# Performance work log

Hardware: AMD Instinct MI355X
Metric: run time of the kernel (lower is better)

Reference implementation:

```python
import jax, jax.numpy as jnp
import numpy as np

NUM_HEADS = 16


def setup_inputs() -> dict:
    key = jax.random.key(0)
    ks = jax.random.split(key, 5)
    b, s, d = 2, 2048, 1024
    std = (2.0 / (d + d)) ** 0.5
    x = jax.random.normal(ks[0], (b, s, d), dtype=jnp.float32)
    Wq = jax.random.normal(ks[1], (d, d), dtype=jnp.float32) * std
    Wk = jax.random.normal(ks[2], (d, d), dtype=jnp.float32) * std
    Wv = jax.random.normal(ks[3], (d, d), dtype=jnp.float32) * std
    Wo = jax.random.normal(ks[4], (d, d), dtype=jnp.float32) * std
    return {"x": x, "Wq": Wq, "Wk": Wk, "Wv": Wv, "Wo": Wo}


def reference(x, Wq, Wk, Wv, Wo):
    b, s, d = x.shape
    h = NUM_HEADS
    dk = d // h
    # projections: bias-free x @ W (W is [in, out])
    def split_heads(t):
        return t.reshape(b, s, h, dk).transpose(0, 2, 1, 3)  # b h s dk
    q = split_heads(x @ Wq)
    k = split_heads(x @ Wk)
    v = split_heads(x @ Wv)
    scale = 1.0 / jnp.sqrt(jnp.asarray(dk, dtype=x.dtype))
    scores = jnp.einsum('bhqd,bhkd->bhqk', q, k) * scale  # b h s s
    causal = jnp.tril(jnp.ones((s, s), dtype=bool))
    scores = jnp.where(causal, scores, -jnp.inf)
    probs = jax.nn.softmax(scores, axis=-1)
    out = jnp.einsum('bhqk,bhkd->bhqd', probs, v)
    out = out.transpose(0, 2, 1, 3).reshape(b, s, d)  # b s (h dk)
    return out @ Wo
```

## Files before the change

### kernel.cpp

```cpp
#include <hip/hip_runtime.h>

typedef unsigned short u16;
typedef unsigned int   u32;

using bf16x8 = __attribute__((ext_vector_type(8))) __bf16;
using bf16x4 = __attribute__((ext_vector_type(4))) __bf16;
using f32x4  = __attribute__((ext_vector_type(4))) float;
using s16x4  = __attribute__((ext_vector_type(4))) short;

#define NH    16
#define DKH   64
#define SEQ   2048
#define BAT   2
#define DMOD  1024

#define QSCALE 0.18033688011112042f

__device__ __forceinline__ u16 f2bf(float f) {
  union { float f; u32 u; } v; v.f = f;
  u32 r = v.u + 0x7fffu + ((v.u >> 16) & 1u);
  return (u16)(r >> 16);
}

__device__ __forceinline__ u32 pack2bf(float a, float b) {
  union { float f; u32 u; } x, y; x.f = a; y.f = b;
  u32 ua = x.u + 0x7fffu + ((x.u >> 16) & 1u);
  u32 ub = y.u + 0x7fffu + ((y.u >> 16) & 1u);
  return __builtin_amdgcn_perm(ub, ua, 0x07060302u);
}

__device__ __forceinline__ s16x4 pk4bf(float a, float b, float c, float d) {
  union { bf16x4 bv; s16x4 sv; } u;
  u.bv[0] = (__bf16)a; u.bv[1] = (__bf16)b; u.bv[2] = (__bf16)c; u.bv[3] = (__bf16)d;
  return u.sv;
}

#if __has_builtin(__builtin_amdgcn_exp2f)
#define EXP2(x) __builtin_amdgcn_exp2f(x)
#else
#define EXP2(x) exp2f(x)
#endif

#if __has_builtin(__builtin_amdgcn_mfma_f32_16x16x16bf16_1k)
__device__ __forceinline__ f32x4 mfma16(s16x4 a, s16x4 b, f32x4 c) {
  return __builtin_amdgcn_mfma_f32_16x16x16bf16_1k(a, b, c, 0, 0, 0);
}
#else
__device__ __forceinline__ f32x4 mfma16(s16x4 a, s16x4 b, f32x4 c) {
  f32x4 d;
  asm volatile("v_mfma_f32_16x16x16_bf16 %0, %1, %2, %3\n\ts_nop 7\n\ts_nop 7"
               : "=v"(d) : "v"(a), "v"(b), "v"(c));
  return d;
}
#endif

typedef const __attribute__((address_space(1))) u32 glb_u32;
typedef __attribute__((address_space(3))) u32 lds_u32;
__device__ __forceinline__ void gload16(const u16* g, u16* l) {
  __builtin_amdgcn_global_load_lds((glb_u32*)(const void*)g, (lds_u32*)(void*)l, 16, 0, 0);
}

__global__ __launch_bounds__(256) void transpose_all(const float* __restrict__ Wq,
                                                     const float* __restrict__ Wk,
                                                     const float* __restrict__ Wv,
                                                     const float* __restrict__ Wo,
                                                     u16* __restrict__ Wt) {
  __shared__ u16 t[32][33];
  const float* W = blockIdx.z == 0 ? Wq : blockIdx.z == 1 ? Wk : blockIdx.z == 2 ? Wv : Wo;
  u16* o = Wt + (size_t)blockIdx.z * DMOD * DMOD;
  int bx = blockIdx.x * 32, by = blockIdx.y * 32;
  int x = threadIdx.x, y = threadIdx.y;
  #pragma unroll
  for (int i = 0; i < 32; i += 8)
    t[y + i][x] = f2bf(W[(size_t)(by + y + i) * DMOD + bx + x]);
  __syncthreads();
  #pragma unroll
  for (int i = 0; i < 32; i += 8)
    o[(size_t)(bx + y + i) * DMOD + by + x] = t[x][y + i];
}

__global__ __launch_bounds__(256) void convert_x(const float* __restrict__ x,
                                                 u16* __restrict__ xb) {
  size_t i = ((size_t)blockIdx.x * 256 + threadIdx.x) * 8;
  float4 f0 = *(const float4*)(x + i);
  float4 f1 = *(const float4*)(x + i + 4);
  uint4 o;
  o.x = pack2bf(f0.x, f0.y); o.y = pack2bf(f0.z, f0.w);
  o.z = pack2bf(f1.x, f1.y); o.w = pack2bf(f1.z, f1.w);
  *(uint4*)(xb + i) = o;
}

__global__ __launch_bounds__(256, 3) void gemm_qkv(const u16* __restrict__ A,
                                                   const u16* __restrict__ Bt,
                                                   u16* __restrict__ Qo,
                                                   u16* __restrict__ Ko,
                                                   u16* __restrict__ Vo) {
  __shared__ __align__(16) u16 As[128 * 32];
  __shared__ __align__(16) u16 Bs[128 * 32];
  const int tid  = threadIdx.x;
  const int lane = tid & 63, wv = tid >> 6;
  const int wm   = wv >> 1, wn = wv & 1;
  const int lrow = lane & 15, quad = lane >> 4;
  const int tileM = blockIdx.x * 128, tileN = blockIdx.y * 128;

  const f32x4 fz = {0.f, 0.f, 0.f, 0.f};
  f32x4 acc[4][4];
  #pragma unroll
  for (int i = 0; i < 4; ++i)
    #pragma unroll
    for (int j = 0; j < 4; ++j) acc[i][j] = fz;

  for (int kt = 0; kt < DMOD; kt += 32) {
    if (kt) __syncthreads();
    #pragma unroll
    for (int i = 0; i < 2; ++i) {
      int idx = i * 256 + tid;
      gload16(&A [(size_t)(tileM + (idx >> 2)) * DMOD + kt + (idx & 3) * 8], &As[idx * 8]);
      gload16(&Bt[(size_t)(tileN + (idx >> 2)) * DMOD + kt + (idx & 3) * 8], &Bs[idx * 8]);
    }
    __syncthreads();

    bf16x8 af[4], bfr[4];
    #pragma unroll
    for (int mt = 0; mt < 4; ++mt)
      af[mt] = *(const bf16x8*)(&As[(wm * 64 + mt * 16 + lrow) * 32 + quad * 8]);
    #pragma unroll
    for (int nt = 0; nt < 4; ++nt)
      bfr[nt] = *(const bf16x8*)(&Bs[(wn * 64 + nt * 16 + lrow) * 32 + quad * 8]);
    #pragma unroll
    for (int mt = 0; mt < 4; ++mt)
      #pragma unroll
      for (int nt = 0; nt < 4; ++nt)
        acc[mt][nt] = __builtin_amdgcn_mfma_f32_16x16x32_bf16(af[mt], bfr[nt],
                                                              acc[mt][nt], 0, 0, 0);
  }

  #pragma unroll
  for (int mt = 0; mt < 4; ++mt) {
    #pragma unroll
    for (int nt = 0; nt < 4; ++nt) {
      int gm0 = tileM + wm * 64 + mt * 16 + quad * 4;
      int gn  = tileN + wn * 64 + nt * 16 + lrow;
      int which = gn >> 10, col = gn & 1023;
      int bb = gm0 >> 11, srw0 = gm0 & (SEQ - 1);
      int hh = col >> 6, dki = col & (DKH - 1);
      size_t bhi = (size_t)(bb * NH + hh);
      if (which == 0) {
        #pragma unroll
        for (int r = 0; r < 4; ++r)
          Qo[(bhi * SEQ + srw0 + r) * DKH + dki] = f2bf(acc[mt][nt][r] * QSCALE);
      } else if (which == 1) {
        #pragma unroll
        for (int r = 0; r < 4; ++r)
          Ko[(bhi * SEQ + srw0 + r) * DKH + dki] = f2bf(acc[mt][nt][r]);
      } else {
        uint2 pk;
        pk.x = pack2bf(acc[mt][nt][0], acc[mt][nt][1]);
        pk.y = pack2bf(acc[mt][nt][2], acc[mt][nt][3]);
        *(uint2*)(&Vo[(((bhi * (SEQ / 4)) + (srw0 >> 2)) * DKH + dki) * 4]) = pk;
      }
    }
  }
}

__global__ __launch_bounds__(256, 3) void gemm_out(const u16* __restrict__ A,
                                                   const u16* __restrict__ Bt,
                                                   float* __restrict__ Co) {
  __shared__ __align__(16) u16 As[128 * 32];
  __shared__ __align__(16) u16 Bs[64 * 32];
  const int tid  = threadIdx.x;
  const int lane = tid & 63, wv = tid >> 6;
  const int wm   = wv & 1, wn = wv >> 1;
  const int lrow = lane & 15, quad = lane >> 4;
  const int tileM = blockIdx.x * 128, tileN = blockIdx.y * 64;

  const f32x4 fz = {0.f, 0.f, 0.f, 0.f};
  f32x4 acc[4][2];
  #pragma unroll
  for (int i = 0; i < 4; ++i) { acc[i][0] = fz; acc[i][1] = fz; }

  for (int kt = 0; kt < DMOD; kt += 32) {
    if (kt) __syncthreads();
    #pragma unroll
    for (int i = 0; i < 2; ++i) {
      int idx = i * 256 + tid;
      gload16(&A[(size_t)(tileM + (idx >> 2)) * DMOD + kt + (idx & 3) * 8], &As[idx * 8]);
    }
    gload16(&Bt[(size_t)(tileN + (tid >> 2)) * DMOD + kt + (tid & 3) * 8], &Bs[tid * 8]);
    __syncthreads();

    bf16x8 af[4], bfr[2];
    #pragma unroll
    for (int mt = 0; mt < 4; ++mt)
      af[mt] = *(const bf16x8*)(&As[(wm * 64 + mt * 16 + lrow) * 32 + quad * 8]);
    #pragma unroll
    for (int nt = 0; nt < 2; ++nt)
      bfr[nt] = *(const bf16x8*)(&Bs[(wn * 32 + nt * 16 + lrow) * 32 + quad * 8]);
    #pragma unroll
    for (int mt = 0; mt < 4; ++mt)
      #pragma unroll
      for (int nt = 0; nt < 2; ++nt)
        acc[mt][nt] = __builtin_amdgcn_mfma_f32_16x16x32_bf16(af[mt], bfr[nt],
                                                              acc[mt][nt], 0, 0, 0);
  }

  #pragma unroll
  for (int mt = 0; mt < 4; ++mt)
    #pragma unroll
    for (int nt = 0; nt < 2; ++nt)
      #pragma unroll
      for (int r = 0; r < 4; ++r) {
        int gm = tileM + wm * 64 + mt * 16 + quad * 4 + r;
        int gn = tileN + wn * 32 + nt * 16 + lrow;
        Co[(size_t)gm * DMOD + gn] = acc[mt][nt][r];
      }
}

#define OPAD 68

__global__ __launch_bounds__(256, 2) void attn_k(const u16* __restrict__ Q,
                                                 const u16* __restrict__ Kg,
                                                 const u16* __restrict__ Vg,
                                                 u16* __restrict__ Og) {
  __shared__ __align__(16) u16 Ksb[2][2][64 * 64];
  __shared__ __align__(16) u16 Vsb[2][2][16 * 256];
  __shared__ __align__(16) u16 Osc[64 * OPAD];
  __shared__ float Lsc[32];

  const int tid  = threadIdx.x;
  const int lane = tid & 63, w = tid >> 6;
  const int g    = w >> 1,  wg = w & 1;
  const int lrow = lane & 15, quad = lane >> 4;
  const int bh = blockIdx.x, y = blockIdx.y;
  const int b = bh >> 4, h = bh & 15;
  const int qB = 31 - y;
  const int sAend = y >> 1;

  const u16* Qbh = Q  + (size_t)bh * SEQ * DKH;
  const u16* Kbh = Kg + (size_t)bh * SEQ * DKH;
  const u16* Vbh = Vg + (size_t)bh * SEQ * DKH;

  const f32x4 fz = {0.f, 0.f, 0.f, 0.f};
  f32x4 oacc[2][4];
  float lsum[2];
  bf16x8 bq[2][2];

#define DEC(s_, g_, qt_, j_, v_)                                                   \
  { if ((s_) <= sAend) { qt_ = y;  j_ = 2 * (s_) + (g_);              v_ = (j_ <= y);  } \
    else               { qt_ = qB; j_ = 2 * ((s_) - sAend - 1) + (g_); v_ = (j_ <= qB); } }

#define STAGE1(gg, p_, j_)                                                          \
  { _Pragma("unroll")                                                               \
    for (int i_ = 0; i_ < 2; ++i_) {                                                \
      int cD = i_ * 256 + tid; int r_ = cD >> 3, c_ = cD & 7;                       \
      gload16(&Kbh[(size_t)((j_) * 64 + r_) * DKH + ((c_ ^ (r_ & 7)) << 3)],        \
              &Ksb[gg][p_][cD * 8]); }                                              \
    _Pragma("unroll")                                                               \
    for (int i_ = 0; i_ < 2; ++i_) {                                                \
      int cD = i_ * 256 + tid; int sq_ = cD >> 5, c_ = cD & 31;                     \
      gload16(&Vbh[(size_t)((j_) * 16 + sq_) * 256 + ((c_ ^ (sq_ & 7)) << 3)],      \
              &Vsb[gg][p_][cD * 8]); } }

#define LOADQ(qt_)                                                                  \
  { _Pragma("unroll")                                                               \
    for (int s_ = 0; s_ < 2; ++s_)                                                  \
      _Pragma("unroll")                                                             \
      for (int kk_ = 0; kk_ < 2; ++kk_)                                             \
        bq[s_][kk_] = *(const bf16x8*)(&Qbh[(size_t)((qt_) * 64 + wg * 32 + s_ * 16 \
                                            + lrow) * DKH + kk_ * 32 + quad * 8]); }

  auto EPI = [&](int qt) {
    float ls[2];
    #pragma unroll
    for (int s2 = 0; s2 < 2; ++s2) {
      float v = lsum[s2];
      v += __shfl_xor(v, 16, 64);
      v += __shfl_xor(v, 32, 64);
      ls[s2] = v;
    }
    float* OscF = (float*)Osc;
    #pragma unroll
    for (int ph = 0; ph < 2; ++ph) {
      if (g == 1) {
        int srow = wg * 16 + lrow;
        #pragma unroll
        for (int d = 0; d < 4; ++d)
          *(f32x4*)(&OscF[srow * OPAD + d * 16 + quad * 4]) = oacc[ph][d];
        if (quad == 0) Lsc[srow] = ls[ph];
      }
      __syncthreads();
      if (g == 0) {
        int srow = wg * 16 + lrow;
        ls[ph] += Lsc[srow];
        #pragma unroll
        for (int d = 0; d < 4; ++d) {
          f32x4 ov = *(const f32x4*)(&OscF[srow * OPAD + d * 16 + quad * 4]);
          oacc[ph][d] += ov;
        }
      }
      __syncthreads();
    }
    if (g == 0) {
      #pragma unroll
      for (int s2 = 0; s2 < 2; ++s2) {
        float inv = 1.f / ls[s2];
        int row = wg * 32 + s2 * 16 + lrow;
        #pragma unroll
        for (int d = 0; d < 4; ++d) {
          uint2 pkk;
          pkk.x = pack2bf(oacc[s2][d][0] * inv, oacc[s2][d][1] * inv);
          pkk.y = pack2bf(oacc[s2][d][2] * inv, oacc[s2][d][3] * inv);
          *(uint2*)(&Osc[row * OPAD + d * 16 + quad * 4]) = pkk;
        }
      }
    }
    __syncthreads();
    #pragma unroll
    for (int k2 = 0; k2 < 2; ++k2) {
      int c2 = k2 * 256 + tid;
      int row = c2 >> 3, ch = c2 & 7;
      uint4 vv = *(const uint4*)(&Osc[row * OPAD + ch * 8]);
      *(uint4*)(&Og[(size_t)(b * SEQ + qt * 64 + row) * DMOD + h * DKH + ch * 8]) = vv;
    }
  };

  { int qt0, j0; bool v0;
    DEC(0, 0, qt0, j0, v0); if (v0) STAGE1(0, 0, j0);
    DEC(0, 1, qt0, j0, v0); if (v0) STAGE1(1, 0, j0);
  }
  LOADQ(y);
  #pragma unroll
  for (int s2 = 0; s2 < 2; ++s2) {
    oacc[s2][0] = fz; oacc[s2][1] = fz; oacc[s2][2] = fz; oacc[s2][3] = fz;
    lsum[s2] = 0.f;
  }
  __syncthreads();

  for (int s = 0; s <= 16; ++s) {
    const int p = s & 1;

    if (s < 16) {
      int qtn, jn; bool vn;
      DEC(s + 1, 0, qtn, jn, vn); if (vn) STAGE1(0, p ^ 1, jn);
      DEC(s + 1, 1, qtn, jn, vn); if (vn) STAGE1(1, p ^ 1, jn);
    }

    int qt, j; bool valid;
    DEC(s, g, qt, j, valid);
    if (valid) {
      const u16* Ks = Ksb[g][p];
      const u16* Vs = Vsb[g][p];
      if (j < qt) {
        __builtin_amdgcn_s_setprio(1);
        f32x4 sacc[2][4];
        #pragma unroll
        for (int s2 = 0; s2 < 2; ++s2)
          #pragma unroll
          for (int m = 0; m < 4; ++m) sacc[s2][m] = fz;
        #pragma unroll
        for (int kk = 0; kk < 2; ++kk)
          #pragma unroll
          for (int m = 0; m < 4; ++m) {
            bf16x8 ak = *(const bf16x8*)(&Ks[(m * 16 + lrow) * 64
                                             + (((kk * 4 + quad) ^ (lrow & 7)) << 3)]);
            sacc[0][m] = __builtin_amdgcn_mfma_f32_16x16x32_bf16(ak, bq[0][kk], sacc[0][m], 0, 0, 0);
            sacc[1][m] = __builtin_amdgcn_mfma_f32_16x16x32_bf16(ak, bq[1][kk], sacc[1][m], 0, 0, 0);
          }
        #pragma unroll
        for (int m = 0; m < 4; ++m) {
          float p00 = EXP2(sacc[0][m][0]), p01 = EXP2(sacc[0][m][1]);
          float p02 = EXP2(sacc[0][m][2]), p03 = EXP2(sacc[0][m][3]);
          float p10 = EXP2(sacc[1][m][0]), p11 = EXP2(sacc[1][m][1]);
          float p12 = EXP2(sacc[1][m][2]), p13 = EXP2(sacc[1][m][3]);
          lsum[0] += (p00 + p01) + (p02 + p03);
          lsum[1] += (p10 + p11) + (p12 + p13);
          s16x4 pk0 = pk4bf(p00, p01, p02, p03);
          s16x4 pk1 = pk4bf(p10, p11, p12, p13);
          const int sq = m * 4 + quad;
          #pragma unroll
          for (int d = 0; d < 4; ++d) {
            int dk = d * 16 + lrow;
            s16x4 av = *(const s16x4*)(&Vs[sq * 256
                                           + ((((dk >> 1) ^ (sq & 7)) << 3) | ((dk & 1) << 2))]);
            oacc[0][d] = mfma16(av, pk0, oacc[0][d]);
            oacc[1][d] = mfma16(av, pk1, oacc[1][d]);
          }
        }
        __builtin_amdgcn_s_setprio(0);
      } else {
        #pragma unroll
        for (int s2 = 0; s2 < 2; ++s2) {
          const int L = 2 * wg + s2;
          for (int m = 0; m < L; ++m) {
            f32x4 sv = fz;
            #pragma unroll
            for (int kk = 0; kk < 2; ++kk) {
              bf16x8 ak = *(const bf16x8*)(&Ks[(m * 16 + lrow) * 64
                                               + (((kk * 4 + quad) ^ (lrow & 7)) << 3)]);
              sv = __builtin_amdgcn_mfma_f32_16x16x32_bf16(ak, bq[s2][kk], sv, 0, 0, 0);
            }
            float p0 = EXP2(sv[0]), p1 = EXP2(sv[1]), p2 = EXP2(sv[2]), p3 = EXP2(sv[3]);
            lsum[s2] += (p0 + p1) + (p2 + p3);
            s16x4 pk = pk4bf(p0, p1, p2, p3);
            const int sq = m * 4 + quad;
            #pragma unroll
            for (int d = 0; d < 4; ++d) {
              int dk = d * 16 + lrow;
              s16x4 av = *(const s16x4*)(&Vs[sq * 256
                                             + ((((dk >> 1) ^ (sq & 7)) << 3) | ((dk & 1) << 2))]);
              oacc[s2][d] = mfma16(av, pk, oacc[s2][d]);
            }
          }
          {
            f32x4 sv = fz;
            #pragma unroll
            for (int kk = 0; kk < 2; ++kk) {
              bf16x8 ak = *(const bf16x8*)(&Ks[(L * 16 + lrow) * 64
                                               + (((kk * 4 + quad) ^ (lrow & 7)) << 3)]);
              sv = __builtin_amdgcn_mfma_f32_16x16x32_bf16(ak, bq[s2][kk], sv, 0, 0, 0);
            }
            float pp[4];
            #pragma unroll
            for (int r = 0; r < 4; ++r)
              pp[r] = (quad * 4 + r > lrow) ? 0.f : EXP2(sv[r]);
            lsum[s2] += (pp[0] + pp[1]) + (pp[2] + pp[3]);
            s16x4 pk = pk4bf(pp[0], pp[1], pp[2], pp[3]);
            const int sq = L * 4 + quad;
            #pragma unroll
            for (int d = 0; d < 4; ++d) {
              int dk = d * 16 + lrow;
              s16x4 av = *(const s16x4*)(&Vs[sq * 256
                                             + ((((dk >> 1) ^ (sq & 7)) << 3) | ((dk & 1) << 2))]);
              oacc[s2][d] = mfma16(av, pk, oacc[s2][d]);
            }
          }
        }
      }
    }

    __syncthreads();

    if (s == sAend) {
      EPI(y);
      #pragma unroll
      for (int s2 = 0; s2 < 2; ++s2) {
        oacc[s2][0] = fz; oacc[s2][1] = fz; oacc[s2][2] = fz; oacc[s2][3] = fz;
        lsum[s2] = 0.f;
      }
      LOADQ(qB);
    } else if (s == 16) {
      EPI(qB);
    }
  }
#undef DEC
#undef STAGE1
#undef LOADQ
}

extern "C" void kernel_launch(void* const* d_in, const int* in_sizes, int n_in,
                              void* d_out, int out_size, void* d_ws, size_t ws_size,
                              hipStream_t stream) {
  const float* x  = (const float*)d_in[0];
  const float* Wq = (const float*)d_in[1];
  const float* Wk = (const float*)d_in[2];
  const float* Wv = (const float*)d_in[3];
  const float* Wo = (const float*)d_in[4];

  u16* ws = (u16*)d_ws;
  const size_t WSZ = (size_t)DMOD * DMOD;
  const size_t TSZ = (size_t)BAT * NH * SEQ * DKH;
  u16* Wt  = ws;
  u16* Wto = Wt + 3 * WSZ;
  u16* xb  = Wt + 4 * WSZ;
  u16* Qb  = xb + TSZ;
  u16* Kb  = Qb + TSZ;
  u16* Vb  = Kb + TSZ;
  u16* Ob  = xb;

  transpose_all<<<dim3(32, 32, 4), dim3(32, 8), 0, stream>>>(Wq, Wk, Wv, Wo, Wt);
  convert_x<<<dim3(2048), 256, 0, stream>>>(x, xb);

  gemm_qkv<<<dim3(32, 24), 256, 0, stream>>>(xb, Wt, Qb, Kb, Vb);

  attn_k<<<dim3(32, 16), 256, 0, stream>>>(Qb, Kb, Vb, Ob);

  gemm_out<<<dim3(32, 16), 256, 0, stream>>>(Ob, Wto, (float*)d_out);
}
```

Baseline: 170.4 us.

## Double GEMM K-tile to 64 with XOR-swizzled LDS layout

Both projection GEMMs now stage 64-wide K slices in shared memory instead of 32, which halves the number of barrier pairs per tile. The LDS layout gains an XOR swizzle on the 16-byte chunk index, applied on global load and on fragment read, to avoid bank conflicts on the wider rows. LDS use per block doubles, which may limit occupancy relative to the launch bound of 3 blocks.

Result: faster. 164.4 us (-3.5%).

```diff
diff --git a/kernel.cpp b/kernel.cpp
--- a/kernel.cpp
+++ b/kernel.cpp
@@ -95,8 +95,8 @@
                                                    u16* __restrict__ Qo,
                                                    u16* __restrict__ Ko,
                                                    u16* __restrict__ Vo) {
-  __shared__ __align__(16) u16 As[128 * 32];
-  __shared__ __align__(16) u16 Bs[128 * 32];
+  __shared__ __align__(16) u16 As[128 * 64];
+  __shared__ __align__(16) u16 Bs[128 * 64];
   const int tid  = threadIdx.x;
   const int lane = tid & 63, wv = tid >> 6;
   const int wm   = wv >> 1, wn = wv & 1;
@@ -110,29 +110,35 @@
     #pragma unroll
     for (int j = 0; j < 4; ++j) acc[i][j] = fz;
 
-  for (int kt = 0; kt < DMOD; kt += 32) {
+  for (int kt = 0; kt < DMOD; kt += 64) {
     if (kt) __syncthreads();
     #pragma unroll
-    for (int i = 0; i < 2; ++i) {
+    for (int i = 0; i < 4; ++i) {
       int idx = i * 256 + tid;
-      gload16(&A [(size_t)(tileM + (idx >> 2)) * DMOD + kt + (idx & 3) * 8], &As[idx * 8]);
-      gload16(&Bt[(size_t)(tileN + (idx >> 2)) * DMOD + kt + (idx & 3) * 8], &Bs[idx * 8]);
+      int r = idx >> 3, c = idx & 7;
+      gload16(&A [(size_t)(tileM + r) * DMOD + kt + ((c ^ (r & 7)) << 3)], &As[idx * 8]);
+      gload16(&Bt[(size_t)(tileN + r) * DMOD + kt + ((c ^ (r & 7)) << 3)], &Bs[idx * 8]);
     }
     __syncthreads();
 
-    bf16x8 af[4], bfr[4];
-    #pragma unroll
-    for (int mt = 0; mt < 4; ++mt)
-      af[mt] = *(const bf16x8*)(&As[(wm * 64 + mt * 16 + lrow) * 32 + quad * 8]);
-    #pragma unroll
-    for (int nt = 0; nt < 4; ++nt)
-      bfr[nt] = *(const bf16x8*)(&Bs[(wn * 64 + nt * 16 + lrow) * 32 + quad * 8]);
-    #pragma unroll
-    for (int mt = 0; mt < 4; ++mt)
+    #pragma unroll
+    for (int kk = 0; kk < 2; ++kk) {
+      bf16x8 af[4], bfr[4];
+      #pragma unroll
+      for (int mt = 0; mt < 4; ++mt)
+        af[mt] = *(const bf16x8*)(&As[(wm * 64 + mt * 16 + lrow) * 64
+                                      + (((kk * 4 + quad) ^ (lrow & 7)) << 3)]);
       #pragma unroll
       for (int nt = 0; nt < 4; ++nt)
-        acc[mt][nt] = __builtin_amdgcn_mfma_f32_16x16x32_bf16(af[mt], bfr[nt],
-                                                              acc[mt][nt], 0, 0, 0);
+        bfr[nt] = *(const bf16x8*)(&Bs[(wn * 64 + nt * 16 + lrow) * 64
+                                       + (((kk * 4 + quad) ^ (lrow & 7)) << 3)]);
+      #pragma unroll
+      for (int mt = 0; mt < 4; ++mt)
+        #pragma unroll
+        for (int nt = 0; nt < 4; ++nt)
+          acc[mt][nt] = __builtin_amdgcn_mfma_f32_16x16x32_bf16(af[mt], bfr[nt],
+                                                                acc[mt][nt], 0, 0, 0);
+    }
   }
 
   #pragma unroll
@@ -166,8 +172,8 @@
 __global__ __launch_bounds__(256, 3) void gemm_out(const u16* __restrict__ A,
                                                    const u16* __restrict__ Bt,
                                                    float* __restrict__ Co) {
-  __shared__ __align__(16) u16 As[128 * 32];
-  __shared__ __align__(16) u16 Bs[64 * 32];
+  __shared__ __align__(16) u16 As[128 * 64];
+  __shared__ __align__(16) u16 Bs[64 * 64];
   const int tid  = threadIdx.x;
   const int lane = tid & 63, wv = tid >> 6;
   const int wm   = wv & 1, wn = wv >> 1;
@@ -179,29 +185,40 @@
   #pragma unroll
   for (int i = 0; i < 4; ++i) { acc[i][0] = fz; acc[i][1] = fz; }
 
-  for (int kt = 0; kt < DMOD; kt += 32) {
+  for (int kt = 0; kt < DMOD; kt += 64) {
     if (kt) __syncthreads();
+    #pragma unroll
+    for (int i = 0; i < 4; ++i) {
+      int idx = i * 256 + tid;
+      int r = idx >> 3, c = idx & 7;
+      gload16(&A[(size_t)(tileM + r) * DMOD + kt + ((c ^ (r & 7)) << 3)], &As[idx * 8]);
+    }
     #pragma unroll
     for (int i = 0; i < 2; ++i) {
       int idx = i * 256 + tid;
-      gload16(&A[(size_t)(tileM + (idx >> 2)) * DMOD + kt + (idx & 3) * 8], &As[idx * 8]);
-    }
-    gload16(&Bt[(size_t)(tileN + (tid >> 2)) * DMOD + kt + (tid & 3) * 8], &Bs[tid * 8]);
+      int r = idx >> 3, c = idx & 7;
+      gload16(&Bt[(size_t)(tileN + r) * DMOD + kt + ((c ^ (r & 7)) << 3)], &Bs[idx * 8]);
+    }
     __syncthreads();
 
-    bf16x8 af[4], bfr[2];
-    #pragma unroll
-    for (int mt = 0; mt < 4; ++mt)
-      af[mt] = *(const bf16x8*)(&As[(wm * 64 + mt * 16 + lrow) * 32 + quad * 8]);
-    #pragma unroll
-    for (int nt = 0; nt < 2; ++nt)
-      bfr[nt] = *(const bf16x8*)(&Bs[(wn * 32 + nt * 16 + lrow) * 32 + quad * 8]);
-    #pragma unroll
-    for (int mt = 0; mt < 4; ++mt)
+    #pragma unroll
+    for (int kk = 0; kk < 2; ++kk) {
+      bf16x8 af[4], bfr[2];
+      #pragma unroll
+      for (int mt = 0; mt < 4; ++mt)
+        af[mt] = *(const bf16x8*)(&As[(wm * 64 + mt * 16 + lrow) * 64
+                                      + (((kk * 4 + quad) ^ (lrow & 7)) << 3)]);
       #pragma unroll
       for (int nt = 0; nt < 2; ++nt)
-        acc[mt][nt] = __builtin_amdgcn_mfma_f32_16x16x32_bf16(af[mt], bfr[nt],
-                                                              acc[mt][nt], 0, 0, 0);
+        bfr[nt] = *(const bf16x8*)(&Bs[(wn * 32 + nt * 16 + lrow) * 64
+                                       + (((kk * 4 + quad) ^ (lrow & 7)) << 3)]);
+      #pragma unroll
+      for (int mt = 0; mt < 4; ++mt)
+        #pragma unroll
+        for (int nt = 0; nt < 2; ++nt)
+          acc[mt][nt] = __builtin_amdgcn_mfma_f32_16x16x32_bf16(af[mt], bfr[nt],
+                                                                acc[mt][nt], 0, 0, 0);
+    }
   }
 
   #pragma unroll
```
